# Performance work log

Measured on AMD Instinct MI355X. Metric: run time of the kernel, lower is better.

## Reference

```python
import jax, jax.numpy as jnp
import numpy as np

N, E = 50000, 500000
A, R, EB, EH, H, C, AH, SH, S, AV = 64, 20, 32, 64, 4, 32, 128, 64, 32, 32
EPS = 1e-8
MAX_DIST = 0.5   # nm, maximum_interaction_radius
SCALE = 1.0      # nm, scale_factor


def physnet_rbf(d):
    # PhysNet radial basis: exp(-beta * (exp(-d) - mu_k)^2), mu_k in [exp(-r_cut), 1]
    mu = jnp.linspace(np.exp(-MAX_DIST), 1.0, R).astype(jnp.float32)
    beta = jnp.float32((2.0 / R * (1.0 - np.exp(-MAX_DIST))) ** -2)
    return jnp.exp(-beta * (jnp.exp(-d)[:, None] - mu) ** 2)  # [E, R]


def _forward(h, x, v, idx_i, idx_j, W_edge_in, b_edge_in, W_edge_h, b_edge_h,
             W_edge_out, b_edge_out, W_att, b_att, W_x_mix, W_node1, b_node1,
             W_node2, b_node2, W_post1, b_post1, W_post2, b_post2,
             W_vel1, b_vel1, W_vel2, w_v_mix):
    n = h.shape[0]
    act = jax.nn.silu
    seg_sum = lambda t, idx: jax.ops.segment_sum(t, idx, num_segments=n)

    # geometry
    r_ij = x[idx_j] - x[idx_i]                       # [E,3]
    d_ij = jnp.sqrt(jnp.sum(r_ij * r_ij, -1) + EPS)  # [E]
    dir_ij = r_ij / (d_ij[:, None] + EPS)            # [E,3]

    # update_edge: gather, RBF filter, edge MLP
    h_cat = jnp.concatenate([h[idx_i], h[idx_j]], -1)                 # [E,2A]
    filtered = physnet_rbf(d_ij) * (h_cat @ W_edge_in + b_edge_in)    # [E,R]
    e_in = jnp.concatenate([h_cat, filtered, d_ij[:, None] / SCALE], -1)
    h_ij_edge = act(e_in @ W_edge_h + b_edge_h) @ W_edge_out + b_edge_out  # [E,EB]

    # semantic attention: CELU logits + segment softmax over receivers per head
    logits = jax.nn.celu(h_ij_edge @ W_att + b_att, alpha=2.0)        # [E,H]
    seg_max = jax.ops.segment_max(logits, idx_i, num_segments=n)      # [n,H]
    exp_l = jnp.exp(logits - seg_max[idx_i])
    denom = seg_sum(exp_l, idx_i)
    att = exp_l / (denom[idx_i] + EPS)                                # [E,H]
    h_ij_semantic = (att[:, :, None] * h_ij_edge[:, None, :]).reshape(-1, H * EB)

    # neighborhood aggregation (scatter-add)
    h_i_semantic = seg_sum(h_ij_semantic, idx_i)                      # [n,H*EB]

    # spatial attention
    mix = jnp.tanh(h_ij_semantic @ W_x_mix)                           # [E,C]
    combinations = dir_ij[:, None, :] * mix[:, :, None]               # [E,C,3]
    counts = jnp.maximum(seg_sum(jnp.ones((idx_i.shape[0],), h.dtype), idx_i), 1.0)
    comb_mean = seg_sum(combinations, idx_i) / counts[:, None, None]  # scatter-mean
    comb_norm2 = jnp.sum(comb_mean * comb_mean, -1)                   # [n,C]
    h_i_spatial = act(act(comb_norm2 @ W_post1 + b_post1) @ W_post2 + b_post2)

    # node update (residual)
    node_in = jnp.concatenate([h, h_i_semantic, h_i_spatial], -1)
    h_upd = h + act(act(node_in @ W_node1 + b_node1) @ W_node2 + b_node2)

    # velocity / coordinate update
    v_ij = jnp.einsum('ecx,c->ex', combinations, w_v_mix)             # [E,3]
    dv = seg_sum(v_ij, idx_i) / counts[:, None]                       # scatter-mean
    gate = 2.0 * jax.nn.sigmoid(act(h_upd @ W_vel1 + b_vel1) @ W_vel2)  # [n,1]
    v_upd = gate * v + dv
    x_upd = x + v_upd
    return h_upd, x_upd, v_upd


def _p(k, shape, scale=0.05):
    return jax.random.normal(k, shape, dtype=jnp.float32) * scale


def setup_inputs() -> dict:
    key = jax.random.key(0)
    ks = jax.random.split(key, 24)
    return {
        'h': jax.random.normal(ks[0], (N, A), dtype=jnp.float32),
        'x': jax.random.normal(ks[1], (N, 3), dtype=jnp.float32),
        'v': jax.random.normal(ks[2], (N, 3), dtype=jnp.float32),
        'idx_i': jax.random.randint(ks[3], (E,), 0, N),
        'idx_j': jax.random.randint(ks[4], (E,), 0, N),
        'W_edge_in': _p(ks[5], (2 * A, R)), 'b_edge_in': jnp.zeros((R,), jnp.float32),
        'W_edge_h': _p(ks[6], (2 * A + R + 1, EH)), 'b_edge_h': jnp.zeros((EH,), jnp.float32),
        'W_edge_out': _p(ks[7], (EH, EB)), 'b_edge_out': jnp.zeros((EB,), jnp.float32),
        'W_att': _p(ks[8], (EB, H)), 'b_att': jnp.zeros((H,), jnp.float32),
        'W_x_mix': _p(ks[9], (H * EB, C)),
        'W_node1': _p(ks[10], (A + H * EB + S, AH)), 'b_node1': jnp.zeros((AH,), jnp.float32),
        'W_node2': _p(ks[11], (AH, A)), 'b_node2': jnp.zeros((A,), jnp.float32),
        'W_post1': _p(ks[12], (C, SH)), 'b_post1': jnp.zeros((SH,), jnp.float32),
        'W_post2': _p(ks[13], (SH, S)), 'b_post2': jnp.zeros((S,), jnp.float32),
        'W_vel1': _p(ks[14], (A, AV)), 'b_vel1': jnp.zeros((AV,), jnp.float32),
        'W_vel2': _p(ks[15], (AV, 1)),
        'w_v_mix': _p(ks[16], (C,)),
    }


def reference(h, x, v, idx_i, idx_j, W_edge_in, b_edge_in, W_edge_h, b_edge_h,
              W_edge_out, b_edge_out, W_att, b_att, W_x_mix, W_node1, b_node1,
              W_node2, b_node2, W_post1, b_post1, W_post2, b_post2,
              W_vel1, b_vel1, W_vel2, w_v_mix):
    return _forward(h, x, v, idx_i, idx_j, W_edge_in, b_edge_in, W_edge_h, b_edge_h,
                    W_edge_out, b_edge_out, W_att, b_att, W_x_mix, W_node1, b_node1,
                    W_node2, b_node2, W_post1, b_post1, W_post2, b_post2,
                    W_vel1, b_vel1, W_vel2, w_v_mix)
```

## Files before the change

### kernel.cpp

```cpp
#include <hip/hip_runtime.h>
#include <math.h>

#define DA 64
#define NODEIN_DIM 224
#define EPSC 1e-8f

typedef short v8s __attribute__((ext_vector_type(8)));
typedef float v4f __attribute__((ext_vector_type(4)));
typedef unsigned short ushort_t;

__device__ __forceinline__ float siluf(float v) {
  return v * __builtin_amdgcn_rcpf(1.0f + __expf(-v));
}
__device__ __forceinline__ float tanhfast(float x) {
  return 1.0f - 2.0f * __builtin_amdgcn_rcpf(__expf(2.0f * x) + 1.0f);
}

__device__ __forceinline__ void atomAddF(float* p, float v) {
#if defined(__HIP_DEVICE_COMPILE__)
  unsafeAtomicAdd(p, v);
#else
  atomicAdd(p, v);
#endif
}

__device__ __forceinline__ unsigned short f2bfu(float f) {
  union { float f; unsigned u; } v; v.f = f;
  unsigned r = v.u + 0x7fffu + ((v.u >> 16) & 1u);
  return (unsigned short)(r >> 16);
}
__device__ __forceinline__ short f2bfs(float f) { return (short)f2bfu(f); }
__device__ __forceinline__ float bf2f(ushort_t s) {
  union { unsigned u; float f; } v; v.u = ((unsigned)s) << 16; return v.f;
}

#define MU0 0.60653065971263342f
#define DMU ((1.0f - 0.60653065971263342f) / 19.0f)
#define BETA ((float)(1.0 / (0.039346934028736658 * 0.039346934028736658)))

__global__ __launch_bounds__(256) void cast_count(
    const float* __restrict__ hsrc, ushort_t* __restrict__ hb, int n4,
    const int* __restrict__ idx_i, int* __restrict__ deg, int E,
    const float* __restrict__ W_node1, ushort_t* __restrict__ W1T)
{
  const int stride = gridDim.x * blockDim.x;
  for (int i = blockIdx.x * blockDim.x + threadIdx.x; i < n4; i += stride) {
    const float4 fv = ((const float4*)hsrc)[i];
    ushort4 o;
    o.x = f2bfu(fv.x); o.y = f2bfu(fv.y); o.z = f2bfu(fv.z); o.w = f2bfu(fv.w);
    ((ushort4*)hb)[i] = o;
  }
  for (int e = blockIdx.x * blockDim.x + threadIdx.x; e < E; e += stride)
    atomicAdd(&deg[idx_i[e]], 1);
  for (int i = blockIdx.x * blockDim.x + threadIdx.x; i < 224 * 128;
       i += stride) {
    const int c = i / 224;
    const int k = i - c * 224;
    W1T[i] = f2bfu(W_node1[k * 128 + c]);
  }
}

#define SCAN_B 64
#define SCAN_T (SCAN_B * 256)

__global__ __launch_bounds__(256) void deg_tsum(
    const int* __restrict__ deg, int* __restrict__ tsum, int N, int C)
{
  const int g = blockIdx.x * blockDim.x + threadIdx.x;
  const int lo = g * C;
  const int hi = (lo + C < N) ? (lo + C) : N;
  int s = 0;
  for (int i = lo; i < hi; ++i) s += deg[i];
  tsum[g] = s;
}

__global__ __launch_bounds__(256) void scan_tsum(int* __restrict__ tsum)
{
  __shared__ int ps[256];
  const int t = threadIdx.x;
  const int per = SCAN_T / 256;
  const int lo = t * per;
  int s = 0;
  for (int i = 0; i < per; ++i) s += tsum[lo + i];
  ps[t] = s;
  __syncthreads();
  if (t == 0) {
    int a = 0;
    for (int i = 0; i < 256; ++i) { const int v = ps[i]; ps[i] = a; a += v; }
  }
  __syncthreads();
  int acc = ps[t];
  for (int i = 0; i < per; ++i) {
    const int v = tsum[lo + i];
    tsum[lo + i] = acc;
    acc += v;
  }
}

__global__ __launch_bounds__(256) void write_csr(
    const int* __restrict__ deg, const int* __restrict__ tpre,
    int* __restrict__ rowstart, int* __restrict__ cursor, int N, int C)
{
  const int g = blockIdx.x * blockDim.x + threadIdx.x;
  const int lo = g * C;
  const int hi = (lo + C < N) ? (lo + C) : N;
  int acc = tpre[g];
  for (int i = lo; i < hi; ++i) {
    const int d = deg[i];
    rowstart[i] = acc;
    cursor[i] = acc;
    acc += d;
  }
  if (hi == N) rowstart[N] = acc;
}

__global__ __launch_bounds__(256) void bucket_edges(
    const int* __restrict__ idx_i, const int* __restrict__ idx_j,
    int* __restrict__ cursor, int2* __restrict__ ijperm, int E)
{
  const int stride = gridDim.x * blockDim.x;
  for (int e = blockIdx.x * blockDim.x + threadIdx.x; e < E; e += stride) {
    const int ii = idx_i[e];
    const int pos = atomicAdd(&cursor[ii], 1);
    ijperm[pos] = make_int2(ii, idx_j[e]);
  }
}

#define THS 72
__global__ __launch_bounds__(256) void edge_f12(
    const ushort_t* __restrict__ h_bf, const float* __restrict__ x,
    const int2* __restrict__ ijperm,
    const float* __restrict__ W_in, const float* __restrict__ b_in,
    const float* __restrict__ W_h, const float* __restrict__ b_h,
    const float* __restrict__ W_out, const float* __restrict__ b_out,
    const float* __restrict__ W_att, const float* __restrict__ b_att,
    float4* __restrict__ dirb, ushort_t* __restrict__ heb,
    float* __restrict__ expl, float* __restrict__ denom, int E)
{
  __shared__ ushort_t sB1[8 * 512];
  __shared__ ushort_t sB2[20 * 512];
  __shared__ ushort_t tH[4][16 * THS];

  const int tid = threadIdx.x;
  for (int idx = tid; idx < 8 * 512; idx += 256) {
    const int j = idx & 7;
    const int ln = (idx >> 3) & 63;
    const int f = idx >> 9;
    const int k = (f >> 1) * 32 + (ln >> 4) * 8 + j;
    const int col = (f & 1) * 16 + (ln & 15);
    sB1[idx] = (col < 20) ? f2bfu(W_in[k * 20 + col]) : (ushort_t)0;
  }
  for (int idx = tid; idx < 20 * 512; idx += 256) {
    const int j = idx & 7;
    const int ln = (idx >> 3) & 63;
    const int f = idx >> 9;
    const int k = (f >> 2) * 32 + (ln >> 4) * 8 + j;
    const int col = (f & 3) * 16 + (ln & 15);
    sB2[idx] = (k < 149) ? f2bfu(W_h[k * 64 + col]) : (ushort_t)0;
  }
  __syncthreads();

  const int gtid = blockIdx.x * blockDim.x + tid;
  const int wid = gtid >> 6;
  const int lane = tid & 63;
  const int w = tid >> 6;
  const int nw = (gridDim.x * blockDim.x) >> 6;
  const int l15 = lane & 15;
  const int q = lane >> 4;

  const ushort_t* b1l = sB1 + lane * 8;
  const ushort_t* b2l = sB2 + lane * 8;

  v8s bfr3[2][2];
  #pragma unroll
  for (int kc = 0; kc < 2; ++kc)
    #pragma unroll
    for (int nt = 0; nt < 2; ++nt)
      #pragma unroll
      for (int j = 0; j < 8; ++j) {
        const int k = kc * 32 + q * 8 + j;
        const int col = nt * 16 + l15;
        bfr3[kc][nt][j] = f2bfs(W_out[k * 32 + col]);
      }

  float bin[2], mu[2];
  #pragma unroll
  for (int nt = 0; nt < 2; ++nt) {
    const int col = nt * 16 + l15;
    bin[nt] = (col < 20) ? b_in[col] : 0.0f;
    mu[nt] = MU0 + (float)col * DMU;
  }
  float bias2[4];
  #pragma unroll
  for (int nt = 0; nt < 4; ++nt) bias2[nt] = b_h[nt * 16 + l15];
  float bias3[2];
  #pragma unroll
  for (int nt = 0; nt < 2; ++nt) bias3[nt] = b_out[nt * 16 + l15];

  v8s battf;
  #pragma unroll
  for (int j = 0; j < 8; ++j)
    battf[j] = (l15 < 4) ? f2bfs(W_att[(q * 8 + j) * 4 + l15]) : (short)0;
  const float bav = (l15 < 4) ? b_att[l15] : 0.0f;

  const int ntiles = (E + 15) >> 4;

  int iiC = 0, jjC = 0;
  v8s afr[4];
  float rCx = 0.f, rCy = 0.f, rCz = 0.f;
  if (wid < ntiles) {
    const int row0 = wid * 16 + l15;
    const int rowL0 = (row0 < E) ? row0 : (E - 1);
    const int2 ij = ijperm[rowL0];
    iiC = ij.x;
    jjC = ij.y;
    afr[0] = *(const v8s*)(h_bf + (size_t)iiC * 64 + q * 8);
    afr[1] = *(const v8s*)(h_bf + (size_t)iiC * 64 + 32 + q * 8);
    afr[2] = *(const v8s*)(h_bf + (size_t)jjC * 64 + q * 8);
    afr[3] = *(const v8s*)(h_bf + (size_t)jjC * 64 + 32 + q * 8);
    if (lane < 16) {
      rCx = x[jjC * 3 + 0] - x[iiC * 3 + 0];
      rCy = x[jjC * 3 + 1] - x[iiC * 3 + 1];
      rCz = x[jjC * 3 + 2] - x[iiC * 3 + 2];
    }
  }

  for (int t = wid; t < ntiles; t += nw) {
    const int tn = t + nw;
    int iiN = 0, jjN = 0;
    v8s nfr[4];
    float rNx = 0.f, rNy = 0.f, rNz = 0.f;
    if (tn < ntiles) {
      const int rowN = tn * 16 + l15;
      const int rowLN = (rowN < E) ? rowN : (E - 1);
      const int2 ij = ijperm[rowLN];
      iiN = ij.x;
      jjN = ij.y;
      nfr[0] = *(const v8s*)(h_bf + (size_t)iiN * 64 + q * 8);
      nfr[1] = *(const v8s*)(h_bf + (size_t)iiN * 64 + 32 + q * 8);
      nfr[2] = *(const v8s*)(h_bf + (size_t)jjN * 64 + q * 8);
      nfr[3] = *(const v8s*)(h_bf + (size_t)jjN * 64 + 32 + q * 8);
      if (lane < 16) {
        rNx = x[jjN * 3 + 0] - x[iiN * 3 + 0];
        rNy = x[jjN * 3 + 1] - x[iiN * 3 + 1];
        rNz = x[jjN * 3 + 2] - x[iiN * 3 + 2];
      }
    }

    const int row = t * 16 + l15;
    float dval = 0.0f;
    if (lane < 16) {
      const float s2 = rCx * rCx + rCy * rCy + rCz * rCz + EPSC;
      const float rv = __builtin_amdgcn_rsqf(s2);
      dval = s2 * rv;
      if (row < E) {
        float4 dq;
        dq.x = rCx * rv; dq.y = rCy * rv; dq.z = rCz * rv; dq.w = dval;
        dirb[row] = dq;
      }
    }

    v4f acc1[2];
    #pragma unroll
    for (int nt = 0; nt < 2; ++nt) {
      v4f a = {0.f, 0.f, 0.f, 0.f};
      #pragma unroll
      for (int kc = 0; kc < 4; ++kc) {
        const v8s bfrag = *(const v8s*)(b1l + (kc * 2 + nt) * 512);
        a = __builtin_amdgcn_mfma_f32_16x16x32_bf16(afr[kc], bfrag, a, 0, 0, 0);
      }
      acc1[nt] = a;
    }

    float dr[4], edr[4];
    #pragma unroll
    for (int r = 0; r < 4; ++r) {
      dr[r] = __shfl(dval, q * 4 + r);
      edr[r] = __expf(-dr[r]);
    }
    #pragma unroll
    for (int nt = 0; nt < 2; ++nt) {
      const int col = nt * 16 + l15;
      #pragma unroll
      for (int r = 0; r < 4; ++r) {
        ushort_t ov;
        if (col < 20) {
          const float tt = edr[r] - mu[nt];
          ov = f2bfu((acc1[nt][r] + bin[nt]) * __expf(-BETA * tt * tt));
        } else if (col == 20) {
          ov = f2bfu(dr[r]);
        } else {
          ov = 0;
        }
        tH[w][(q * 4 + r) * THS + col] = ov;
      }
    }
    __builtin_amdgcn_wave_barrier();

    const v8s afr4 = *(const v8s*)&tH[w][l15 * THS + q * 8];
    __builtin_amdgcn_wave_barrier();

    v4f acc2[4];
    #pragma unroll
    for (int nt = 0; nt < 4; ++nt) {
      v4f a = {0.f, 0.f, 0.f, 0.f};
      #pragma unroll
      for (int kc = 0; kc < 4; ++kc) {
        const v8s bfrag = *(const v8s*)(b2l + (kc * 4 + nt) * 512);
        a = __builtin_amdgcn_mfma_f32_16x16x32_bf16(afr[kc], bfrag, a, 0, 0, 0);
      }
      const v8s bfrag4 = *(const v8s*)(b2l + (4 * 4 + nt) * 512);
      a = __builtin_amdgcn_mfma_f32_16x16x32_bf16(afr4, bfrag4, a, 0, 0, 0);
      acc2[nt] = a;
    }

    #pragma unroll
    for (int nt = 0; nt < 4; ++nt) {
      #pragma unroll
      for (int r = 0; r < 4; ++r)
        tH[w][(q * 4 + r) * THS + nt * 16 + l15] =
            f2bfu(siluf(acc2[nt][r] + bias2[nt]));
    }
    __builtin_amdgcn_wave_barrier();

    v8s af3[2];
    af3[0] = *(const v8s*)&tH[w][l15 * THS + q * 8];
    af3[1] = *(const v8s*)&tH[w][l15 * THS + 32 + q * 8];

    v4f acc3[2];
    #pragma unroll
    for (int nt = 0; nt < 2; ++nt) {
      v4f a = {0.f, 0.f, 0.f, 0.f};
      #pragma unroll
      for (int kc = 0; kc < 2; ++kc)
        a = __builtin_amdgcn_mfma_f32_16x16x32_bf16(af3[kc], bfr3[kc][nt], a, 0, 0, 0);
      acc3[nt] = a;
    }
    __builtin_amdgcn_wave_barrier();

    const int rowb = t * 16 + q * 4;
    #pragma unroll
    for (int nt = 0; nt < 2; ++nt) {
      const int col = nt * 16 + l15;
      #pragma unroll
      for (int r = 0; r < 4; ++r) {
        const ushort_t hv = f2bfu(acc3[nt][r] + bias3[nt]);
        tH[w][(q * 4 + r) * THS + col] = hv;
        if (rowb + r < E) heb[(size_t)(rowb + r) * 32 + col] = hv;
      }
    }
    __builtin_amdgcn_wave_barrier();

    const v8s afA = *(const v8s*)&tH[w][l15 * THS + q * 8];
    v4f az = {0.f, 0.f, 0.f, 0.f};
    const v4f aacc = __builtin_amdgcn_mfma_f32_16x16x32_bf16(afA, battf, az, 0, 0, 0);

    int ii_r[4];
    #pragma unroll
    for (int r = 0; r < 4; ++r) ii_r[r] = __shfl(iiC, q * 4 + r);

    if (l15 < 4) {
      #pragma unroll
      for (int r = 0; r < 4; ++r) {
        if (rowb + r < E) {
          const float la = aacc[r] + bav;
          const float l = (la > 0.f) ? la : 2.0f * (__expf(0.5f * la) - 1.0f);
          const float ev = __expf(l);
          expl[(size_t)(rowb + r) * 4 + l15] = ev;
          atomAddF(&denom[ii_r[r] * 4 + l15], ev);
        }
      }
    }
    __builtin_amdgcn_wave_barrier();

    iiC = iiN; jjC = jjN;
    afr[0] = nfr[0]; afr[1] = nfr[1]; afr[2] = nfr[2]; afr[3] = nfr[3];
    rCx = rNx; rCy = rNy; rCz = rNz;
  }
}

__global__ __launch_bounds__(256) void node_fused(
    const int* __restrict__ rowstart,
    const ushort_t* __restrict__ heb,
    const float* __restrict__ expl, const float* __restrict__ denom,
    const float4* __restrict__ dirb,
    const float* __restrict__ W_xmix, const float* __restrict__ w_vmix,
    ushort_t* __restrict__ hsem, float* __restrict__ norm2,
    float* __restrict__ dv_mean, int N)
{
  __shared__ ushort_t sBX[8 * 512];

  const int tid = threadIdx.x;
  for (int idx = tid; idx < 8 * 512; idx += 256) {
    const int j = idx & 7;
    const int ln = (idx >> 3) & 63;
    const int f = idx >> 9;
    const int k = (f >> 1) * 32 + (ln >> 4) * 8 + j;
    const int col = (f & 1) * 16 + (ln & 15);
    sBX[idx] = f2bfu(W_xmix[k * 32 + col]);
  }
  __syncthreads();

  const int gtid = blockIdx.x * blockDim.x + tid;
  const int wid = gtid >> 6;
  const int lane = tid & 63;
  const int nw = (gridDim.x * blockDim.x) >> 6;
  const int l15 = lane & 15;
  const int q = lane >> 4;
  const ushort_t* bXl = sBX + lane * 8;

  const float wv0 = w_vmix[l15];
  const float wv1 = w_vmix[16 + l15];

  int sC = 0, eC = 0;
  if (wid < N) {
    sC = rowstart[wid];
    eC = rowstart[wid + 1];
  }

  for (int n = wid; n < N; n += nw) {
    const int nn = n + nw;
    int sN = 0, eN = 0;
    if (nn < N) {
      sN = rowstart[nn];
      eN = rowstart[nn + 1];
    }
    const int s = sC;
    const int epd = eC;
    const int deg = epd - s;

    const float4 dnm = *(const float4*)(denom + n * 4);
    float invden[4];
    invden[0] = __builtin_amdgcn_rcpf(dnm.x + EPSC);
    invden[1] = __builtin_amdgcn_rcpf(dnm.y + EPSC);
    invden[2] = __builtin_amdgcn_rcpf(dnm.z + EPSC);
    invden[3] = __builtin_amdgcn_rcpf(dnm.w + EPSC);

    {
      float sm00 = 0.f, sm01 = 0.f, sm10 = 0.f, sm11 = 0.f;
      float sm20 = 0.f, sm21 = 0.f, sm30 = 0.f, sm31 = 0.f;
      int k = s;
      for (; k + 4 <= epd; k += 4) {
        const unsigned hv = ((const unsigned*)heb)[k * 16 + lane];
        const float4 ex = ((const float4*)expl)[k + q];
        const float h0 = bf2f((ushort_t)(hv & 0xffffu));
        const float h1 = bf2f((ushort_t)(hv >> 16));
        sm00 += ex.x * h0; sm01 += ex.x * h1;
        sm10 += ex.y * h0; sm11 += ex.y * h1;
        sm20 += ex.z * h0; sm21 += ex.z * h1;
        sm30 += ex.w * h0; sm31 += ex.w * h1;
      }
      if (k < epd) {
        const int ke = k + q;
        const int kl = (ke < epd) ? ke : (epd - 1);
        const float live = (ke < epd) ? 1.0f : 0.0f;
        const unsigned hv = ((const unsigned*)heb)[kl * 16 + l15];
        const float4 ex = ((const float4*)expl)[kl];
        const float h0 = bf2f((ushort_t)(hv & 0xffffu)) * live;
        const float h1 = bf2f((ushort_t)(hv >> 16)) * live;
        sm00 += ex.x * h0; sm01 += ex.x * h1;
        sm10 += ex.y * h0; sm11 += ex.y * h1;
        sm20 += ex.z * h0; sm21 += ex.z * h1;
        sm30 += ex.w * h0; sm31 += ex.w * h1;
      }
      sm00 += __shfl_xor(sm00, 16); sm00 += __shfl_xor(sm00, 32);
      sm01 += __shfl_xor(sm01, 16); sm01 += __shfl_xor(sm01, 32);
      sm10 += __shfl_xor(sm10, 16); sm10 += __shfl_xor(sm10, 32);
      sm11 += __shfl_xor(sm11, 16); sm11 += __shfl_xor(sm11, 32);
      sm20 += __shfl_xor(sm20, 16); sm20 += __shfl_xor(sm20, 32);
      sm21 += __shfl_xor(sm21, 16); sm21 += __shfl_xor(sm21, 32);
      sm30 += __shfl_xor(sm30, 16); sm30 += __shfl_xor(sm30, 32);
      sm31 += __shfl_xor(sm31, 16); sm31 += __shfl_xor(sm31, 32);
      const float sa = (q & 2) ? ((q & 1) ? sm30 : sm20)
                               : ((q & 1) ? sm10 : sm00);
      const float sb = (q & 2) ? ((q & 1) ? sm31 : sm21)
                               : ((q & 1) ? sm11 : sm01);
      const float idn = (q & 2) ? ((q & 1) ? invden[3] : invden[2])
                                : ((q & 1) ? invden[1] : invden[0]);
      const unsigned pack = (unsigned)f2bfu(sa * idn) |
                            ((unsigned)f2bfu(sb * idn) << 16);
      ((unsigned*)hsem)[n * 64 + lane] = pack;
    }

    float cx0 = 0.f, cy0 = 0.f, cz0 = 0.f;
    float cx1 = 0.f, cy1 = 0.f, cz1 = 0.f;

    for (int c0 = 0; c0 < deg; c0 += 16) {
      const int ra = c0 + l15;
      const int eA = s + ((ra < deg) ? ra : (deg - 1));
      const v8s hech = *(const v8s*)(heb + eA * 32 + q * 8);

      v4f y[4][2];
      #pragma unroll
      for (int h4 = 0; h4 < 4; ++h4) {
        #pragma unroll
        for (int nt = 0; nt < 2; ++nt) {
          v4f z = {0.f, 0.f, 0.f, 0.f};
          y[h4][nt] = __builtin_amdgcn_mfma_f32_16x16x32_bf16(
              hech, *(const v8s*)(bXl + (h4 * 2 + nt) * 512), z, 0, 0, 0);
        }
      }

      #pragma unroll
      for (int r = 0; r < 4; ++r) {
        const int rr = c0 + q * 4 + r;
        const int live = rr < deg;
        const int eR = s + (live ? rr : (deg - 1));
        const float lf = live ? 1.0f : 0.0f;
        const float4 ex4 = *(const float4*)(expl + eR * 4);
        const float at0 = ex4.x * invden[0] * lf;
        const float at1 = ex4.y * invden[1] * lf;
        const float at2 = ex4.z * invden[2] * lf;
        const float at3 = ex4.w * invden[3] * lf;
        const float p0 = at0 * y[0][0][r] + at1 * y[1][0][r] +
                         at2 * y[2][0][r] + at3 * y[3][0][r];
        const float p1 = at0 * y[0][1][r] + at1 * y[1][1][r] +
                         at2 * y[2][1][r] + at3 * y[3][1][r];
        const float4 dq = dirb[eR];
        const float m0 = tanhfast(p0);
        const float m1 = tanhfast(p1);
        cx0 += dq.x * m0; cy0 += dq.y * m0; cz0 += dq.z * m0;
        cx1 += dq.x * m1; cy1 += dq.y * m1; cz1 += dq.z * m1;
      }
    }

    cx0 += __shfl_xor(cx0, 16); cx0 += __shfl_xor(cx0, 32);
    cy0 += __shfl_xor(cy0, 16); cy0 += __shfl_xor(cy0, 32);
    cz0 += __shfl_xor(cz0, 16); cz0 += __shfl_xor(cz0, 32);
    cx1 += __shfl_xor(cx1, 16); cx1 += __shfl_xor(cx1, 32);
    cy1 += __shfl_xor(cy1, 16); cy1 += __shfl_xor(cy1, 32);
    cz1 += __shfl_xor(cz1, 16); cz1 += __shfl_xor(cz1, 32);

    const float cinv = __builtin_amdgcn_rcpf(fmaxf((float)deg, 1.0f));

    if (lane < 32) {
      const float mx = ((lane & 16) ? cx1 : cx0) * cinv;
      const float my = ((lane & 16) ? cy1 : cy0) * cinv;
      const float mz = ((lane & 16) ? cz1 : cz0) * cinv;
      norm2[n * 32 + lane] = mx * mx + my * my + mz * mz;
    }

    float tx = wv0 * cx0 + wv1 * cx1;
    float ty = wv0 * cy0 + wv1 * cy1;
    float tz = wv0 * cz0 + wv1 * cz1;
    tx += __shfl_xor(tx, 1); tx += __shfl_xor(tx, 2);
    tx += __shfl_xor(tx, 4); tx += __shfl_xor(tx, 8);
    ty += __shfl_xor(ty, 1); ty += __shfl_xor(ty, 2);
    ty += __shfl_xor(ty, 4); ty += __shfl_xor(ty, 8);
    tz += __shfl_xor(tz, 1); tz += __shfl_xor(tz, 2);
    tz += __shfl_xor(tz, 4); tz += __shfl_xor(tz, 8);
    if (lane == 0) {
      dv_mean[n * 3 + 0] = tx * cinv;
      dv_mean[n * 3 + 1] = ty * cinv;
      dv_mean[n * 3 + 2] = tz * cinv;
    }

    sC = sN; eC = eN;
  }
}

__global__ __launch_bounds__(256) void node_c1_mfma(
    const ushort_t* __restrict__ h_bf, const ushort_t* __restrict__ hsem,
    const float* __restrict__ norm2, const ushort_t* __restrict__ W1T,
    const float* __restrict__ W_post1, const float* __restrict__ b_post1,
    const float* __restrict__ W_post2, const float* __restrict__ b_post2,
    const float* __restrict__ b_node1,
    ushort_t* __restrict__ nh_out, int N)
{
  __shared__ ushort_t tp[4][16 * THS];

  const int tid = threadIdx.x;
  const int lane = tid & 63;
  const int w = tid >> 6;
  const int l15 = lane & 15;
  const int q = lane >> 4;

  v8s bp1[4];
  #pragma unroll
  for (int nt = 0; nt < 4; ++nt)
    #pragma unroll
    for (int j = 0; j < 8; ++j)
      bp1[nt][j] = f2bfs(W_post1[(q * 8 + j) * 64 + nt * 16 + l15]);
  v8s bp2[2][2];
  #pragma unroll
  for (int kc = 0; kc < 2; ++kc)
    #pragma unroll
    for (int nt = 0; nt < 2; ++nt)
      #pragma unroll
      for (int j = 0; j < 8; ++j)
        bp2[kc][nt][j] = f2bfs(W_post2[(kc * 32 + q * 8 + j) * 32 + nt * 16 + l15]);
  float bb1[4];
  #pragma unroll
  for (int nt = 0; nt < 4; ++nt) bb1[nt] = b_post1[nt * 16 + l15];
  float bb2[2];
  #pragma unroll
  for (int nt = 0; nt < 2; ++nt) bb2[nt] = b_post2[nt * 16 + l15];
  float b1[8];
  #pragma unroll
  for (int nt = 0; nt < 8; ++nt) b1[nt] = b_node1[nt * 16 + l15];

  const ushort_t* w1base = W1T + l15 * 224 + q * 8;

  const int gw = blockIdx.x * 4 + w;
  const int nwv = gridDim.x * 4;
  const int ntiles = (N + 15) >> 4;

  for (int t = gw; t < ntiles; t += nwv) {
    const int row = t * 16 + l15;
    const int rowL = (row < N) ? row : (N - 1);

    const float4 nA = *(const float4*)(norm2 + (size_t)rowL * 32 + q * 8);
    const float4 nB = *(const float4*)(norm2 + (size_t)rowL * 32 + q * 8 + 4);
    v8s a1;
    a1[0] = f2bfs(nA.x); a1[1] = f2bfs(nA.y);
    a1[2] = f2bfs(nA.z); a1[3] = f2bfs(nA.w);
    a1[4] = f2bfs(nB.x); a1[5] = f2bfs(nB.y);
    a1[6] = f2bfs(nB.z); a1[7] = f2bfs(nB.w);

    v4f p1[4];
    #pragma unroll
    for (int nt = 0; nt < 4; ++nt) {
      v4f a = {0.f, 0.f, 0.f, 0.f};
      p1[nt] = __builtin_amdgcn_mfma_f32_16x16x32_bf16(a1, bp1[nt], a, 0, 0, 0);
    }
    #pragma unroll
    for (int nt = 0; nt < 4; ++nt)
      #pragma unroll
      for (int r = 0; r < 4; ++r)
        tp[w][(q * 4 + r) * THS + nt * 16 + l15] =
            f2bfu(siluf(p1[nt][r] + bb1[nt]));
    __builtin_amdgcn_wave_barrier();

    v8s a2[2];
    a2[0] = *(const v8s*)&tp[w][l15 * THS + q * 8];
    a2[1] = *(const v8s*)&tp[w][l15 * THS + 32 + q * 8];

    v4f p2[2];
    #pragma unroll
    for (int nt = 0; nt < 2; ++nt) {
      v4f a = {0.f, 0.f, 0.f, 0.f};
      #pragma unroll
      for (int kc = 0; kc < 2; ++kc)
        a = __builtin_amdgcn_mfma_f32_16x16x32_bf16(a2[kc], bp2[kc][nt], a, 0, 0, 0);
      p2[nt] = a;
    }
    __builtin_amdgcn_wave_barrier();
    #pragma unroll
    for (int nt = 0; nt < 2; ++nt)
      #pragma unroll
      for (int r = 0; r < 4; ++r)
        tp[w][(q * 4 + r) * THS + nt * 16 + l15] =
            f2bfu(siluf(p2[nt][r] + bb2[nt]));
    __builtin_amdgcn_wave_barrier();

    v8s af[7];
    af[0] = *(const v8s*)(h_bf + (size_t)rowL * 64 + q * 8);
    af[1] = *(const v8s*)(h_bf + (size_t)rowL * 64 + 32 + q * 8);
    #pragma unroll
    for (int kc = 0; kc < 4; ++kc)
      af[2 + kc] = *(const v8s*)(hsem + (size_t)rowL * 128 + kc * 32 + q * 8);
    af[6] = *(const v8s*)&tp[w][l15 * THS + q * 8];

    v4f acc[8];
    #pragma unroll
    for (int nt = 0; nt < 8; ++nt) acc[nt] = (v4f){0.f, 0.f, 0.f, 0.f};
    #pragma unroll
    for (int kc = 0; kc < 7; ++kc) {
      #pragma unroll
      for (int nt = 0; nt < 8; ++nt) {
        const v8s bfrag = *(const v8s*)(w1base + nt * 16 * 224 + kc * 32);
        acc[nt] = __builtin_amdgcn_mfma_f32_16x16x32_bf16(af[kc], bfrag, acc[nt], 0, 0, 0);
      }
    }

    const int rowb = t * 16 + q * 4;
    #pragma unroll
    for (int nt = 0; nt < 8; ++nt) {
      #pragma unroll
      for (int r = 0; r < 4; ++r)
        if (rowb + r < N)
          nh_out[(size_t)(rowb + r) * 128 + nt * 16 + l15] =
              f2bfu(siluf(acc[nt][r] + b1[nt]));
    }
  }
}

__global__ __launch_bounds__(256) void node_c2_mfma(
    const float* __restrict__ h, const float* __restrict__ x,
    const float* __restrict__ v, const ushort_t* __restrict__ nh,
    const float* __restrict__ dv_mean,
    const float* __restrict__ W_node2, const float* __restrict__ b_node2,
    const float* __restrict__ W_vel1, const float* __restrict__ b_vel1,
    const float* __restrict__ W_vel2,
    float* __restrict__ out, int N)
{
  __shared__ ushort_t sW2[16 * 64 * 8];
  __shared__ ushort_t sWv[4 * 64 * 8];
  __shared__ ushort_t tH[4][16 * THS];
  __shared__ float sg[4][16];

  const int tid = threadIdx.x;
  for (int idx = tid; idx < 16 * 64 * 8; idx += 256) {
    const int j = idx & 7;
    const int ln = (idx >> 3) & 63;
    const int f = idx >> 9;
    const int k = (f >> 2) * 32 + (ln >> 4) * 8 + j;
    const int col = (f & 3) * 16 + (ln & 15);
    sW2[idx] = f2bfu(W_node2[k * 64 + col]);
  }
  for (int idx = tid; idx < 4 * 64 * 8; idx += 256) {
    const int j = idx & 7;
    const int ln = (idx >> 3) & 63;
    const int f = idx >> 9;
    const int k = (f >> 1) * 32 + (ln >> 4) * 8 + j;
    const int col = (f & 1) * 16 + (ln & 15);
    sWv[idx] = f2bfu(W_vel1[k * 32 + col]);
  }
  __syncthreads();

  const int lane = tid & 63;
  const int w = tid >> 6;
  const int l15 = lane & 15;
  const int q = lane >> 4;

  const ushort_t* w2l = sW2 + lane * 8;
  const ushort_t* wvl = sWv + lane * 8;

  float b2[4];
  #pragma unroll
  for (int nt = 0; nt < 4; ++nt) b2[nt] = b_node2[nt * 16 + l15];
  float bv[2];
  #pragma unroll
  for (int nt = 0; nt < 2; ++nt) bv[nt] = b_vel1[nt * 16 + l15];
  float wv2[2];
  #pragma unroll
  for (int nt = 0; nt < 2; ++nt) wv2[nt] = W_vel2[nt * 16 + l15];

  const int gw = blockIdx.x * 4 + w;
  const int nwv = gridDim.x * 4;
  const int ntiles = (N + 15) >> 4;

  for (int t = gw; t < ntiles; t += nwv) {
    const int row = t * 16 + l15;
    const int rowL = (row < N) ? row : (N - 1);

    v8s af[4];
    #pragma unroll
    for (int kc = 0; kc < 4; ++kc)
      af[kc] = *(const v8s*)(nh + (size_t)rowL * 128 + kc * 32 + q * 8);

    v4f acc[4];
    #pragma unroll
    for (int nt = 0; nt < 4; ++nt) {
      v4f a = {0.f, 0.f, 0.f, 0.f};
      #pragma unroll
      for (int kc = 0; kc < 4; ++kc) {
        const v8s bfrag = *(const v8s*)(w2l + (kc * 4 + nt) * 512);
        a = __builtin_amdgcn_mfma_f32_16x16x32_bf16(af[kc], bfrag, a, 0, 0, 0);
      }
      acc[nt] = a;
    }

    const int rowb = t * 16 + q * 4;
    #pragma unroll
    for (int nt = 0; nt < 4; ++nt) {
      const int col = nt * 16 + l15;
      #pragma unroll
      for (int r = 0; r < 4; ++r) {
        const int n = rowb + r;
        if (n < N) {
          const float hu = h[(size_t)n * 64 + col] + siluf(acc[nt][r] + b2[nt]);
          out[(size_t)n * 64 + col] = hu;
          tH[w][(q * 4 + r) * THS + col] = f2bfu(hu);
        }
      }
    }
    __builtin_amdgcn_wave_barrier();

    v8s a2[2];
    a2[0] = *(const v8s*)&tH[w][l15 * THS + q * 8];
    a2[1] = *(const v8s*)&tH[w][l15 * THS + 32 + q * 8];
    v4f av[2];
    #pragma unroll
    for (int nt = 0; nt < 2; ++nt) {
      v4f a = {0.f, 0.f, 0.f, 0.f};
      #pragma unroll
      for (int kc = 0; kc < 2; ++kc) {
        const v8s bfrag = *(const v8s*)(wvl + (kc * 2 + nt) * 512);
        a = __builtin_amdgcn_mfma_f32_16x16x32_bf16(a2[kc], bfrag, a, 0, 0, 0);
      }
      av[nt] = a;
    }

    #pragma unroll
    for (int r = 0; r < 4; ++r) {
      float pr = siluf(av[0][r] + bv[0]) * wv2[0] +
                 siluf(av[1][r] + bv[1]) * wv2[1];
      pr += __shfl_xor(pr, 1);
      pr += __shfl_xor(pr, 2);
      pr += __shfl_xor(pr, 4);
      pr += __shfl_xor(pr, 8);
      if (l15 == 0)
        sg[w][q * 4 + r] = 2.0f * __builtin_amdgcn_rcpf(1.0f + __expf(-pr));
    }
    __builtin_amdgcn_wave_barrier();

    if (lane < 48) {
      const int rr = lane / 3;
      const int c = lane % 3;
      const int n = t * 16 + rr;
      if (n < N) {
        const float gate = sg[w][rr];
        const float dv = dv_mean[n * 3 + c];
        const float vu = gate * v[n * 3 + c] + dv;
        out[(size_t)N * 64 + (size_t)n * 3 + c] = x[n * 3 + c] + vu;
        out[(size_t)N * 64 + (size_t)N * 3 + (size_t)n * 3 + c] = vu;
      }
    }
    __builtin_amdgcn_wave_barrier();
  }
}

extern "C" void kernel_launch(void* const* d_in, const int* in_sizes, int n_in,
                              void* d_out, int out_size, void* d_ws, size_t ws_size,
                              hipStream_t stream) {
  const float* h   = (const float*)d_in[0];
  const float* x   = (const float*)d_in[1];
  const float* v   = (const float*)d_in[2];
  const int* idx_i = (const int*)d_in[3];
  const int* idx_j = (const int*)d_in[4];
  const float* W_edge_in  = (const float*)d_in[5];
  const float* b_edge_in  = (const float*)d_in[6];
  const float* W_edge_h   = (const float*)d_in[7];
  const float* b_edge_h   = (const float*)d_in[8];
  const float* W_edge_out = (const float*)d_in[9];
  const float* b_edge_out = (const float*)d_in[10];
  const float* W_att      = (const float*)d_in[11];
  const float* b_att      = (const float*)d_in[12];
  const float* W_x_mix    = (const float*)d_in[13];
  const float* W_node1    = (const float*)d_in[14];
  const float* b_node1    = (const float*)d_in[15];
  const float* W_node2    = (const float*)d_in[16];
  const float* b_node2    = (const float*)d_in[17];
  const float* W_post1    = (const float*)d_in[18];
  const float* b_post1    = (const float*)d_in[19];
  const float* W_post2    = (const float*)d_in[20];
  const float* b_post2    = (const float*)d_in[21];
  const float* W_vel1     = (const float*)d_in[22];
  const float* b_vel1     = (const float*)d_in[23];
  const float* W_vel2     = (const float*)d_in[24];
  const float* w_v_mix    = (const float*)d_in[25];

  const int E = in_sizes[3];
  const int N = in_sizes[0] / DA;

  float* ws = (float*)d_ws;
  size_t off = 0;
  float* denom    = ws + off; off += (size_t)N * 4;
  int*   deg      = (int*)(ws + off); off += (size_t)N;
  const size_t zeroBytes = off * sizeof(float);
  int*   rowstart = (int*)(ws + off); off += (size_t)N + 4;
  int*   cursor   = (int*)(ws + off); off += (size_t)N;
  int*   tsum     = (int*)(ws + off); off += (size_t)SCAN_T;
  int2*  ijperm   = (int2*)(ws + off); off += (size_t)E * 2;
  float* expl     = ws + off; off += (size_t)E * 4;
  float* dirbR    = ws + off; off += (size_t)E * 4;
  float* hsemR    = ws + off; off += (size_t)N * 64;
  float* norm2    = ws + off; off += (size_t)N * 32;
  float* dv_mean  = ws + off; off += (size_t)N * 4;
  float* hbfR     = ws + off; off += (size_t)N * 32;
  float* w1tR     = ws + off; off += (size_t)14336;
  float* fltR     = ws + off; off += (size_t)E * 16;
  float* hebR     = ws + off; off += (size_t)E * 16;

  ushort_t* h_bf = (ushort_t*)hbfR;
  ushort_t* hsem = (ushort_t*)hsemR;
  ushort_t* heb  = (ushort_t*)hebR;
  ushort_t* nh   = (ushort_t*)fltR;
  ushort_t* W1T  = (ushort_t*)w1tR;
  float4*   dirb = (float4*)dirbR;

  hipMemsetAsync(d_ws, 0, zeroBytes, stream);

  {
    const int n4 = (N * 64) / 4;
    cast_count<<<1024, 256, 0, stream>>>(h, h_bf, n4, idx_i, deg, E,
                                         W_node1, W1T);
  }
  {
    const int C = (N + SCAN_T - 1) / SCAN_T;
    deg_tsum<<<SCAN_B, 256, 0, stream>>>(deg, tsum, N, C);
    scan_tsum<<<1, 256, 0, stream>>>(tsum);
    write_csr<<<SCAN_B, 256, 0, stream>>>(deg, tsum, rowstart, cursor, N, C);
  }
  bucket_edges<<<512, 256, 0, stream>>>(idx_i, idx_j, cursor, ijperm, E);
  edge_f12<<<1024, 256, 0, stream>>>(h_bf, x, ijperm,
                                     W_edge_in, b_edge_in, W_edge_h, b_edge_h,
                                     W_edge_out, b_edge_out, W_att, b_att,
                                     dirb, heb, expl, denom, E);
  node_fused<<<2048, 256, 0, stream>>>(rowstart, heb, expl, denom, dirb,
                                       W_x_mix, w_v_mix, hsem, norm2,
                                       dv_mean, N);
  node_c1_mfma<<<784, 256, 0, stream>>>(
      h_bf, hsem, norm2, W1T, W_post1, b_post1, W_post2, b_post2,
      b_node1, nh, N);
  node_c2_mfma<<<784, 256, 0, stream>>>(
      h, x, v, nh, dv_mean, W_node2, b_node2, W_vel1, b_vel1, W_vel2,
      (float*)d_out, N);
}
```

Baseline: 373.4 us.

## Fuse node MLP stages into one kernel and pre-swizzle W_node1 fragments

Merges the two node-side MFMA kernels into a single kernel. The hidden activation tile now passes through per-wave shared memory in two halves instead of being written to and re-read from a global bf16 buffer, which removes one launch and that global round-trip. W_node1 is also pre-laid out in MFMA fragment order, so each lane's B-fragment load is contiguous across lanes. In exchange the fused kernel uses more registers and shared memory, which may lower occupancy.

Result: no change. 377.8 us (+1.2%).

```diff
diff --git a/kernel.cpp b/kernel.cpp
--- a/kernel.cpp
+++ b/kernel.cpp
@@ -2,7 +2,6 @@
 #include <math.h>
 
 #define DA 64
-#define NODEIN_DIM 224
 #define EPSC 1e-8f
 
 typedef short v8s __attribute__((ext_vector_type(8)));
@@ -41,7 +40,7 @@
 __global__ __launch_bounds__(256) void cast_count(
     const float* __restrict__ hsrc, ushort_t* __restrict__ hb, int n4,
     const int* __restrict__ idx_i, int* __restrict__ deg, int E,
-    const float* __restrict__ W_node1, ushort_t* __restrict__ W1T)
+    const float* __restrict__ W_node1, ushort_t* __restrict__ W1F)
 {
   const int stride = gridDim.x * blockDim.x;
   for (int i = blockIdx.x * blockDim.x + threadIdx.x; i < n4; i += stride) {
@@ -52,11 +51,16 @@
   }
   for (int e = blockIdx.x * blockDim.x + threadIdx.x; e < E; e += stride)
     atomicAdd(&deg[idx_i[e]], 1);
-  for (int i = blockIdx.x * blockDim.x + threadIdx.x; i < 224 * 128;
-       i += stride) {
-    const int c = i / 224;
-    const int k = i - c * 224;
-    W1T[i] = f2bfu(W_node1[k * 128 + c]);
+  for (int idx = blockIdx.x * blockDim.x + threadIdx.x; idx < 7 * 8 * 512;
+       idx += stride) {
+    const int j = idx & 7;
+    const int ln = (idx >> 3) & 63;
+    const int f = idx >> 9;
+    const int kc = f >> 3;
+    const int nt = f & 7;
+    const int k = kc * 32 + (ln >> 4) * 8 + j;
+    const int c = nt * 16 + (ln & 15);
+    W1F[idx] = f2bfu(W_node1[k * 128 + c]);
   }
 }
 
@@ -559,22 +563,52 @@
   }
 }
 
-__global__ __launch_bounds__(256) void node_c1_mfma(
+__global__ __launch_bounds__(256) void node_c12(
     const ushort_t* __restrict__ h_bf, const ushort_t* __restrict__ hsem,
-    const float* __restrict__ norm2, const ushort_t* __restrict__ W1T,
+    const float* __restrict__ norm2, const ushort_t* __restrict__ W1F,
     const float* __restrict__ W_post1, const float* __restrict__ b_post1,
     const float* __restrict__ W_post2, const float* __restrict__ b_post2,
     const float* __restrict__ b_node1,
-    ushort_t* __restrict__ nh_out, int N)
+    const float* __restrict__ h, const float* __restrict__ x,
+    const float* __restrict__ v, const float* __restrict__ dv_mean,
+    const float* __restrict__ W_node2, const float* __restrict__ b_node2,
+    const float* __restrict__ W_vel1, const float* __restrict__ b_vel1,
+    const float* __restrict__ W_vel2,
+    float* __restrict__ out, int N)
 {
+  __shared__ ushort_t sW2[16 * 512];
+  __shared__ ushort_t sWv[4 * 512];
   __shared__ ushort_t tp[4][16 * THS];
+  __shared__ float sg[4][16];
 
   const int tid = threadIdx.x;
+  for (int idx = tid; idx < 16 * 512; idx += 256) {
+    const int j = idx & 7;
+    const int ln = (idx >> 3) & 63;
+    const int f = idx >> 9;
+    const int k = (f >> 2) * 32 + (ln >> 4) * 8 + j;
+    const int col = (f & 3) * 16 + (ln & 15);
+    sW2[idx] = f2bfu(W_node2[k * 64 + col]);
+  }
+  for (int idx = tid; idx < 4 * 512; idx += 256) {
+    const int j = idx & 7;
+    const int ln = (idx >> 3) & 63;
+    const int f = idx >> 9;
+    const int k = (f >> 1) * 32 + (ln >> 4) * 8 + j;
+    const int col = (f & 1) * 16 + (ln & 15);
+    sWv[idx] = f2bfu(W_vel1[k * 32 + col]);
+  }
+  __syncthreads();
+
   const int lane = tid & 63;
   const int w = tid >> 6;
   const int l15 = lane & 15;
   const int q = lane >> 4;
 
+  const ushort_t* w2l = sW2 + lane * 8;
+  const ushort_t* wvl = sWv + lane * 8;
+  const ushort_t* w1l = W1F + lane * 8;
+
   v8s bp1[4];
   #pragma unroll
   for (int nt = 0; nt < 4; ++nt)
@@ -598,8 +632,15 @@
   float b1[8];
   #pragma unroll
   for (int nt = 0; nt < 8; ++nt) b1[nt] = b_node1[nt * 16 + l15];
-
-  const ushort_t* w1base = W1T + l15 * 224 + q * 8;
+  float b2[4];
+  #pragma unroll
+  for (int nt = 0; nt < 4; ++nt) b2[nt] = b_node2[nt * 16 + l15];
+  float bv[2];
+  #pragma unroll
+  for (int nt = 0; nt < 2; ++nt) bv[nt] = b_vel1[nt * 16 + l15];
+  float wv2[2];
+  #pragma unroll
+  for (int nt = 0; nt < 2; ++nt) wv2[nt] = W_vel2[nt * 16 + l15];
 
   const int gw = blockIdx.x * 4 + w;
   const int nwv = gridDim.x * 4;
@@ -668,97 +709,44 @@
     for (int kc = 0; kc < 7; ++kc) {
       #pragma unroll
       for (int nt = 0; nt < 8; ++nt) {
-        const v8s bfrag = *(const v8s*)(w1base + nt * 16 * 224 + kc * 32);
+        const v8s bfrag = *(const v8s*)(w1l + (kc * 8 + nt) * 512);
         acc[nt] = __builtin_amdgcn_mfma_f32_16x16x32_bf16(af[kc], bfrag, acc[nt], 0, 0, 0);
       }
     }
 
-    const int rowb = t * 16 + q * 4;
-    #pragma unroll
-    for (int nt = 0; nt < 8; ++nt) {
+    __builtin_amdgcn_wave_barrier();
+    #pragma unroll
+    for (int nt = 0; nt < 4; ++nt)
       #pragma unroll
       for (int r = 0; r < 4; ++r)
-        if (rowb + r < N)
-          nh_out[(size_t)(rowb + r) * 128 + nt * 16 + l15] =
-              f2bfu(siluf(acc[nt][r] + b1[nt]));
-    }
-  }
-}
-
-__global__ __launch_bounds__(256) void node_c2_mfma(
-    const float* __restrict__ h, const float* __restrict__ x,
-    const float* __restrict__ v, const ushort_t* __restrict__ nh,
-    const float* __restrict__ dv_mean,
-    const float* __restrict__ W_node2, const float* __restrict__ b_node2,
-    const float* __restrict__ W_vel1, const float* __restrict__ b_vel1,
-    const float* __restrict__ W_vel2,
-    float* __restrict__ out, int N)
-{
-  __shared__ ushort_t sW2[16 * 64 * 8];
-  __shared__ ushort_t sWv[4 * 64 * 8];
-  __shared__ ushort_t tH[4][16 * THS];
-  __shared__ float sg[4][16];
-
-  const int tid = threadIdx.x;
-  for (int idx = tid; idx < 16 * 64 * 8; idx += 256) {
-    const int j = idx & 7;
-    const int ln = (idx >> 3) & 63;
-    const int f = idx >> 9;
-    const int k = (f >> 2) * 32 + (ln >> 4) * 8 + j;
-    const int col = (f & 3) * 16 + (ln & 15);
-    sW2[idx] = f2bfu(W_node2[k * 64 + col]);
-  }
-  for (int idx = tid; idx < 4 * 64 * 8; idx += 256) {
-    const int j = idx & 7;
-    const int ln = (idx >> 3) & 63;
-    const int f = idx >> 9;
-    const int k = (f >> 1) * 32 + (ln >> 4) * 8 + j;
-    const int col = (f & 1) * 16 + (ln & 15);
-    sWv[idx] = f2bfu(W_vel1[k * 32 + col]);
-  }
-  __syncthreads();
-
-  const int lane = tid & 63;
-  const int w = tid >> 6;
-  const int l15 = lane & 15;
-  const int q = lane >> 4;
-
-  const ushort_t* w2l = sW2 + lane * 8;
-  const ushort_t* wvl = sWv + lane * 8;
-
-  float b2[4];
-  #pragma unroll
-  for (int nt = 0; nt < 4; ++nt) b2[nt] = b_node2[nt * 16 + l15];
-  float bv[2];
-  #pragma unroll
-  for (int nt = 0; nt < 2; ++nt) bv[nt] = b_vel1[nt * 16 + l15];
-  float wv2[2];
-  #pragma unroll
-  for (int nt = 0; nt < 2; ++nt) wv2[nt] = W_vel2[nt * 16 + l15];
-
-  const int gw = blockIdx.x * 4 + w;
-  const int nwv = gridDim.x * 4;
-  const int ntiles = (N + 15) >> 4;
-
-  for (int t = gw; t < ntiles; t += nwv) {
-    const int row = t * 16 + l15;
-    const int rowL = (row < N) ? row : (N - 1);
-
-    v8s af[4];
-    #pragma unroll
-    for (int kc = 0; kc < 4; ++kc)
-      af[kc] = *(const v8s*)(nh + (size_t)rowL * 128 + kc * 32 + q * 8);
-
-    v4f acc[4];
+        tp[w][(q * 4 + r) * THS + nt * 16 + l15] =
+            f2bfu(siluf(acc[nt][r] + b1[nt]));
+    __builtin_amdgcn_wave_barrier();
+    v8s af2[4];
+    af2[0] = *(const v8s*)&tp[w][l15 * THS + q * 8];
+    af2[1] = *(const v8s*)&tp[w][l15 * THS + 32 + q * 8];
+    __builtin_amdgcn_wave_barrier();
+    #pragma unroll
+    for (int nt = 4; nt < 8; ++nt)
+      #pragma unroll
+      for (int r = 0; r < 4; ++r)
+        tp[w][(q * 4 + r) * THS + (nt - 4) * 16 + l15] =
+            f2bfu(siluf(acc[nt][r] + b1[nt]));
+    __builtin_amdgcn_wave_barrier();
+    af2[2] = *(const v8s*)&tp[w][l15 * THS + q * 8];
+    af2[3] = *(const v8s*)&tp[w][l15 * THS + 32 + q * 8];
+    __builtin_amdgcn_wave_barrier();
+
+    v4f accB[4];
     #pragma unroll
     for (int nt = 0; nt < 4; ++nt) {
       v4f a = {0.f, 0.f, 0.f, 0.f};
       #pragma unroll
       for (int kc = 0; kc < 4; ++kc) {
         const v8s bfrag = *(const v8s*)(w2l + (kc * 4 + nt) * 512);
-        a = __builtin_amdgcn_mfma_f32_16x16x32_bf16(af[kc], bfrag, a, 0, 0, 0);
-      }
-      acc[nt] = a;
+        a = __builtin_amdgcn_mfma_f32_16x16x32_bf16(af2[kc], bfrag, a, 0, 0, 0);
+      }
+      accB[nt] = a;
     }
 
     const int rowb = t * 16 + q * 4;
@@ -769,17 +757,17 @@
       for (int r = 0; r < 4; ++r) {
         const int n = rowb + r;
         if (n < N) {
-          const float hu = h[(size_t)n * 64 + col] + siluf(acc[nt][r] + b2[nt]);
+          const float hu = h[(size_t)n * 64 + col] + siluf(accB[nt][r] + b2[nt]);
           out[(size_t)n * 64 + col] = hu;
-          tH[w][(q * 4 + r) * THS + col] = f2bfu(hu);
+          tp[w][(q * 4 + r) * THS + col] = f2bfu(hu);
         }
       }
     }
     __builtin_amdgcn_wave_barrier();
 
-    v8s a2[2];
-    a2[0] = *(const v8s*)&tH[w][l15 * THS + q * 8];
-    a2[1] = *(const v8s*)&tH[w][l15 * THS + 32 + q * 8];
+    v8s a3[2];
+    a3[0] = *(const v8s*)&tp[w][l15 * THS + q * 8];
+    a3[1] = *(const v8s*)&tp[w][l15 * THS + 32 + q * 8];
     v4f av[2];
     #pragma unroll
     for (int nt = 0; nt < 2; ++nt) {
@@ -787,7 +775,7 @@
       #pragma unroll
       for (int kc = 0; kc < 2; ++kc) {
         const v8s bfrag = *(const v8s*)(wvl + (kc * 2 + nt) * 512);
-        a = __builtin_amdgcn_mfma_f32_16x16x32_bf16(a2[kc], bfrag, a, 0, 0, 0);
+        a = __builtin_amdgcn_mfma_f32_16x16x32_bf16(a3[kc], bfrag, a, 0, 0, 0);
       }
       av[nt] = a;
     }
@@ -869,15 +857,13 @@
   float* norm2    = ws + off; off += (size_t)N * 32;
   float* dv_mean  = ws + off; off += (size_t)N * 4;
   float* hbfR     = ws + off; off += (size_t)N * 32;
-  float* w1tR     = ws + off; off += (size_t)14336;
-  float* fltR     = ws + off; off += (size_t)E * 16;
+  float* w1fR     = ws + off; off += (size_t)14336;
   float* hebR     = ws + off; off += (size_t)E * 16;
 
   ushort_t* h_bf = (ushort_t*)hbfR;
   ushort_t* hsem = (ushort_t*)hsemR;
   ushort_t* heb  = (ushort_t*)hebR;
-  ushort_t* nh   = (ushort_t*)fltR;
-  ushort_t* W1T  = (ushort_t*)w1tR;
+  ushort_t* W1F  = (ushort_t*)w1fR;
   float4*   dirb = (float4*)dirbR;
 
   hipMemsetAsync(d_ws, 0, zeroBytes, stream);
@@ -885,7 +871,7 @@
   {
     const int n4 = (N * 64) / 4;
     cast_count<<<1024, 256, 0, stream>>>(h, h_bf, n4, idx_i, deg, E,
-                                         W_node1, W1T);
+                                         W_node1, W1F);
   }
   {
     const int C = (N + SCAN_T - 1) / SCAN_T;
@@ -901,10 +887,8 @@
   node_fused<<<2048, 256, 0, stream>>>(rowstart, heb, expl, denom, dirb,
                                        W_x_mix, w_v_mix, hsem, norm2,
                                        dv_mean, N);
-  node_c1_mfma<<<784, 256, 0, stream>>>(
-      h_bf, hsem, norm2, W1T, W_post1, b_post1, W_post2, b_post2,
-      b_node1, nh, N);
-  node_c2_mfma<<<784, 256, 0, stream>>>(
-      h, x, v, nh, dv_mean, W_node2, b_node2, W_vel1, b_vel1, W_vel2,
+  node_c12<<<784, 256, 0, stream>>>(
+      h_bf, hsem, norm2, W1F, W_post1, b_post1, W_post2, b_post2, b_node1,
+      h, x, v, dv_mean, W_node2, b_node2, W_vel1, b_vel1, W_vel2,
       (float*)d_out, N);
 }
```
